# Kernel tuning notes

Measured on AMD Instinct MI355X. Metric: run time of the kernel, lower is better.

## Reference

```python
import jax, jax.numpy as jnp
import numpy as np

D_STATE = 16; D_MODEL = 256; N_HEADS = 8; N_LAYERS = 4; D_REL = 64
HEALTH = 0
WORLD = (1024.0, 1024.0)
B, T, N = 32, 512, 8
ACTION_DIM = 12


def setup_inputs() -> dict:
    key = jax.random.key(0)
    ks = iter(jax.random.split(key, 48))
    s = 0.02
    def w(shape):
        return jax.random.normal(next(ks), shape, jnp.float32) * s
    inp = dict(
        state=jax.random.normal(next(ks), (B, T, N, D_STATE), jnp.float32),
        pos=jax.random.uniform(next(ks), (B, T, N, 2), jnp.float32),
        vel=jax.random.normal(next(ks), (B, T, N, 2), jnp.float32),
        team_ids=jax.random.randint(next(ks), (B, T, N), 0, 2, jnp.int32),
        alive=jax.random.randint(next(ks), (B, T, N), 0, 2, jnp.int32).astype(bool),
        dead=jnp.zeros((D_STATE,), jnp.float32),
        enc_W1=w((D_STATE, D_MODEL)), enc_b1=jnp.zeros((D_MODEL,), jnp.float32),
        enc_W2=w((D_MODEL, D_MODEL)), enc_b2=jnp.zeros((D_MODEL,), jnp.float32),
        team_emb=w((2, D_MODEL)), ship_emb=w((8, D_MODEL)),
        trunk_W1=w((6, D_REL)), trunk_b1=jnp.zeros((D_REL,), jnp.float32),
        trunk_W2=w((D_REL, D_REL)), trunk_b2=jnp.zeros((D_REL,), jnp.float32),
        adapt_W=w((N_LAYERS, D_REL, N_HEADS)), adapt_b=jnp.zeros((N_LAYERS, N_HEADS), jnp.float32),
        norm_w=jnp.ones((N_LAYERS, D_MODEL), jnp.float32),
        Wq=w((N_LAYERS, D_MODEL, D_MODEL)), bq=jnp.zeros((N_LAYERS, D_MODEL), jnp.float32),
        Wk=w((N_LAYERS, D_MODEL, D_MODEL)), bk=jnp.zeros((N_LAYERS, D_MODEL), jnp.float32),
        Wv=w((N_LAYERS, D_MODEL, D_MODEL)), bv=jnp.zeros((N_LAYERS, D_MODEL), jnp.float32),
        Wo=w((N_LAYERS, D_MODEL, D_MODEL)), bo=jnp.zeros((N_LAYERS, D_MODEL), jnp.float32),
        head_W=w((D_MODEL, ACTION_DIM)), head_b=jnp.zeros((ACTION_DIM,), jnp.float32),
    )
    return inp


def _rms(x, g, eps=1e-6):
    return x * jax.lax.rsqrt(jnp.mean(x * x, axis=-1, keepdims=True) + eps) * g


def reference(state, pos, vel, team_ids, alive, dead,
              enc_W1, enc_b1, enc_W2, enc_b2, team_emb, ship_emb,
              trunk_W1, trunk_b1, trunk_W2, trunk_b2, adapt_W, adapt_b,
              norm_w, Wq, bq, Wk, bk, Wv, bv, Wo, bo, head_W, head_b):
    ws = jnp.asarray(WORLD, state.dtype)
    # replace dead entities' state with learned 'dead' vector
    state = jnp.where(alive[..., None], state, dead)
    # state encoder (MLP)
    h = jax.nn.silu(state @ enc_W1 + enc_b1) @ enc_W2 + enc_b2
    # special embeddings
    h = h + team_emb[team_ids] + ship_emb[jnp.arange(N)]  # ship_emb broadcasts over B,T
    # relational trunk: pairwise toroidal geometry features [B,T,N,N,6]
    p = pos * ws
    rel = p[:, :, :, None, :] - p[:, :, None, :, :]
    rel = rel - jnp.round(rel / ws) * ws  # toroidal wrap
    relv = vel[:, :, :, None, :] - vel[:, :, None, :, :]
    dn = jnp.sqrt(jnp.sum(rel * rel, axis=-1) + 1e-8) / ws[0]
    feats = jnp.concatenate([rel / ws, relv, dn[..., None], 1.0 / (1.0 + dn[..., None])], axis=-1)
    trunk = jax.nn.silu(feats @ trunk_W1 + trunk_b1) @ trunk_W2 + trunk_b2  # [B,T,N,N,D_REL]
    dh = D_MODEL // N_HEADS
    scale = dh ** -0.5
    kmask = alive[:, :, None, None, :]  # mask keys
    x = h
    for i in range(N_LAYERS):
        nx = _rms(x, norm_w[i])
        # adapter: per-layer relational bias [B,T,H,N,N]
        bias = jnp.transpose(trunk @ adapt_W[i] + adapt_b[i], (0, 1, 4, 2, 3))
        q = (nx @ Wq[i] + bq[i]).reshape(B, T, N, N_HEADS, dh)
        k = (nx @ Wk[i] + bk[i]).reshape(B, T, N, N_HEADS, dh)
        v = (nx @ Wv[i] + bv[i]).reshape(B, T, N, N_HEADS, dh)
        sc = jnp.einsum('btihd,btjhd->bthij', q, k) * scale + bias
        sc = jnp.where(kmask, sc, -1e9)
        a = jax.nn.softmax(sc, axis=-1)
        o = jnp.einsum('bthij,btjhd->btihd', a, v).reshape(B, T, N, D_MODEL)
        x = x + o @ Wo[i] + bo[i]
    action_logits = x @ head_W + head_b  # [B,T,N,12]
    return action_logits
```

## Files before the change

### kernel.cpp

```cpp
#include <hip/hip_runtime.h>
#include <cstdint>

#define DEV __device__ __forceinline__

typedef __attribute__((ext_vector_type(8))) short short8;
typedef __attribute__((ext_vector_type(4))) float floatx4;
typedef unsigned short u16;
typedef unsigned int u32;

DEV u16 f2bf(float f) {
    unsigned u = __float_as_uint(f);
    return (u16)((u + 0x7fffu + ((u >> 16) & 1u)) >> 16);
}
DEV void unpack2(u32 u, float& a, float& b) {
    a = __uint_as_float(u << 16);
    b = __uint_as_float(u & 0xffff0000u);
}
DEV u32 pack2f(float a, float b) { return (u32)f2bf(a) | ((u32)f2bf(b) << 16); }
DEV float sigm(float x) { return 1.0f / (1.0f + __expf(-x)); }

#define NAG 8
#define DM 256
#define NL 4
#define AD 12
#define MROWS 64
#define NBLK 2048
#define THREADS 512

#define OFF_E1   0
#define OFF_E2   8192
#define OFF_QKVO 73728
#define OFF_TW2  1122304
#define OFF_ADW  1126400
#define WS_TOTAL 1128448
#define WS_BYTES (WS_TOTAL * 2)

#define L_R1    0
#define L_KB    33792
#define L_V     67584
#define L_R2    101376
#define L_RED   135168
#define L_SPOS  137216
#define L_SVEL  137728
#define SMEM_BYTES 138240

#define TRK(row, col) ((row) * 64 + ((((col) >> 3) ^ ((row) & 7)) << 3) + ((col) & 7))

enum { I_STATE=0, I_POS, I_VEL, I_TEAM, I_ALIVE, I_DEAD, I_EW1, I_EB1, I_EW2, I_EB2,
       I_TEMB, I_SEMB, I_TW1, I_TB1, I_TW2, I_TB2, I_ADW, I_ADB, I_NORMW,
       I_WQ, I_BQ, I_WK, I_BK, I_WV, I_BV, I_WO, I_BO, I_HW, I_HB, N_IN };

struct Args { const void* in[N_IN]; float* out; };

__global__ __launch_bounds__(256) void prep_kernel(Args a, u16* ws)
{
    int e = blockIdx.x * 256 + threadIdx.x;
    int mat = blockIdx.y;
    int size, offs, N, Kreal;
    const float* src;
    if (mat == 0)      { size = 8192;  offs = OFF_E1;  N = 256; Kreal = 16;  src = (const float*)a.in[I_EW1]; }
    else if (mat == 1) { size = 65536; offs = OFF_E2;  N = 256; Kreal = 256; src = (const float*)a.in[I_EW2]; }
    else if (mat < 18) {
        int q = mat - 2, l = q >> 2, m = q & 3;
        int wi = (m == 0) ? I_WQ : (m == 1) ? I_WK : (m == 2) ? I_WV : I_WO;
        size = 65536; offs = OFF_QKVO + q * 65536; N = 256; Kreal = 256;
        src = (const float*)a.in[wi] + l * 65536;
    }
    else if (mat == 18) { size = 4096; offs = OFF_TW2; N = 64; Kreal = 64; src = (const float*)a.in[I_TW2]; }
    else                { size = 2048; offs = OFF_ADW; N = 32; Kreal = 64; src = (const float*)a.in[I_ADW]; }
    if (e >= size) return;
    int ksblk = N * 32;
    int ks = e / ksblk, rem = e % ksblk;
    int n = rem >> 5, quad = (rem >> 3) & 3, j = rem & 7;
    int k = ks * 32 + quad * 8 + j;
    float v = 0.0f;
    if (k < Kreal) {
        if (mat == 19) v = src[((n >> 3) * 64 + k) * 8 + (n & 7)];
        else           v = src[k * N + n];
    }
    ws[offs + e] = f2bf(v);
}

DEV short8 ld_u4(const u16* p) {
    return __builtin_bit_cast(short8, *(const uint4*)p);
}
DEV short8 ld_afrag(const u16* A, int stride, int row0, int kofs, int l15, int quad) {
    return ld_u4(A + (row0 + l15) * stride + kofs + quad * 8);
}
DEV short8 ld_bws(const u16* w, int ksblk, int ks, int col, int l15, int quad) {
    return ld_u4(w + ks * ksblk + (col + l15) * 32 + quad * 8);
}
DEV short8 ld_bf32(const float* W, int N, int Kreal, int ks, int col, int l15, int quad) {
    short8 r;
    #pragma unroll
    for (int j = 0; j < 8; j++) {
        int k = ks * 32 + quad * 8 + j;
        float v = (k < Kreal) ? W[k * N + col + l15] : 0.0f;
        r[j] = (short)f2bf(v);
    }
    return r;
}

template<bool UW>
DEV void gemm64(const u16* A, const u16* wsW, const float* Wf,
                int Kb, int Kreal, int colw, int l15, int quad, floatx4 acc[4][2]) {
    #pragma unroll 2
    for (int ks = 0; ks < Kb; ks++) {
        short8 af[4];
        #pragma unroll
        for (int mi = 0; mi < 4; mi++)
            af[mi] = ld_afrag(A, 264, mi * 16, ks * 32, l15, quad);
        short8 bf[2];
        #pragma unroll
        for (int nj = 0; nj < 2; nj++)
            bf[nj] = UW ? ld_bws(wsW, 8192, ks, colw + nj * 16, l15, quad)
                        : ld_bf32(Wf, 256, Kreal, ks, colw + nj * 16, l15, quad);
        #pragma unroll
        for (int mi = 0; mi < 4; mi++)
            #pragma unroll
            for (int nj = 0; nj < 2; nj++)
                acc[mi][nj] = __builtin_amdgcn_mfma_f32_16x16x32_bf16(af[mi], bf[nj], acc[mi][nj], 0, 0, 0);
    }
}

template<bool UW>
__global__ __launch_bounds__(THREADS, 2) void yemong_mfma(Args a, const u16* ws)
{
    extern __shared__ char smem[];
    u16* sR1   = (u16*)(smem + L_R1);
    u16* skb   = (u16*)(smem + L_KB);
    u16* sV    = (u16*)(smem + L_V);
    u16* sR2   = (u16*)(smem + L_R2);
    float* sred = (float*)(smem + L_RED);
    float* spos = (float*)(smem + L_SPOS);
    float* svel = (float*)(smem + L_SVEL);

    const int t = threadIdx.x, bid = blockIdx.x;
    const int lane = t & 63, w = t >> 6;
    const int l15 = lane & 15, quad = lane >> 4;
    const int colw = w * 32;
    const int rowt = w * 64;
    const int p = w >> 1, h0 = (w & 1) * 4;

    float xr[4][2][4];
    u32 br[NL][4][2];
    u32 amask;

    unsigned mp = 0;
    const unsigned* au = (const unsigned*)a.in[I_ALIVE];
    #pragma unroll
    for (int i = 0; i < 16; i++) mp |= au[i];
    const bool abyte = (mp > 1u);
    auto aliveAt = [&](int r) -> int {
        int gi = bid * MROWS + r;
        return abyte ? (int)((const unsigned char*)a.in[I_ALIVE])[gi]
                     : ((const int*)a.in[I_ALIVE])[gi];
    };
    auto rms_partials = [&]() {
        float ssv[16];
        #pragma unroll
        for (int mi = 0; mi < 4; mi++)
            #pragma unroll
            for (int r = 0; r < 4; r++) {
                float x0 = xr[mi][0][r], x1 = xr[mi][1][r];
                ssv[mi * 4 + r] = fmaf(x0, x0, x1 * x1);
            }
        #pragma unroll
        for (int m = 1; m < 16; m <<= 1)
            #pragma unroll
            for (int k2 = 0; k2 < 16; k2++) ssv[k2] += __shfl_xor(ssv[k2], m);
        if (l15 == 0) {
            #pragma unroll
            for (int mi = 0; mi < 4; mi++)
                #pragma unroll
                for (int r = 0; r < 4; r++)
                    sred[(mi * 16 + quad * 4 + r) * 8 + w] = ssv[mi * 4 + r];
        }
    };

    if (t < 128) {
        int n = t >> 1, d = t & 1;
        spos[n * 2 + d] = ((const float*)a.in[I_POS])[(bid * MROWS + n) * 2 + d] * 1024.0f;
        svel[n * 2 + d] = ((const float*)a.in[I_VEL])[(bid * MROWS + n) * 2 + d];
    }
    {
        int tk = 2 * p + (quad >> 1);
        amask = 0;
        #pragma unroll
        for (int j = 0; j < 8; j++) amask |= (aliveAt(tk * 8 + j) ? 1u : 0u) << j;
    }
    {
        const float* gs = (const float*)a.in[I_STATE];
        const float* gd = (const float*)a.in[I_DEAD];
        #pragma unroll
        for (int it = 0; it < 4; it++) {
            int idx = t + THREADS * it;
            int r = idx >> 5, kk = idx & 31;
            float v = 0.0f;
            if (kk < 16) v = aliveAt(r) ? gs[(bid * MROWS + r) * 16 + kk] : gd[kk];
            sR2[r * 264 + kk] = f2bf(v);
        }
    }
    __syncthreads();

    {
        floatx4 acc[4][2] = {};
        gemm64<UW>(sR2, ws + OFF_E1, (const float*)a.in[I_EW1], 1, 16, colw, l15, quad, acc);
        __syncthreads();
        const float* b1 = (const float*)a.in[I_EB1];
        #pragma unroll
        for (int nj = 0; nj < 2; nj++) {
            int c = colw + nj * 16 + l15;
            float bb = b1[c];
            #pragma unroll
            for (int mi = 0; mi < 4; mi++)
                #pragma unroll
                for (int r = 0; r < 4; r++) {
                    float v = acc[mi][nj][r] + bb;
                    sR2[(mi * 16 + quad * 4 + r) * 264 + c] = f2bf(v * sigm(v));
                }
        }
    }
    __syncthreads();

    {
        floatx4 acc[4][2] = {};
        gemm64<UW>(sR2, ws + OFF_E2, (const float*)a.in[I_EW2], 8, 256, colw, l15, quad, acc);
        const float* b2 = (const float*)a.in[I_EB2];
        const float* te = (const float*)a.in[I_TEMB];
        const float* se = (const float*)a.in[I_SEMB];
        const int* gteam = (const int*)a.in[I_TEAM];
        int team16[16];
        #pragma unroll
        for (int mi = 0; mi < 4; mi++)
            #pragma unroll
            for (int r = 0; r < 4; r++)
                team16[mi * 4 + r] = gteam[bid * MROWS + mi * 16 + quad * 4 + r];
        #pragma unroll
        for (int nj = 0; nj < 2; nj++) {
            int c = colw + nj * 16 + l15;
            float bb = b2[c];
            #pragma unroll
            for (int mi = 0; mi < 4; mi++)
                #pragma unroll
                for (int r = 0; r < 4; r++) {
                    int row = mi * 16 + quad * 4 + r;
                    xr[mi][nj][r] = acc[mi][nj][r] + bb + te[team16[mi * 4 + r] * 256 + c] + se[(row & 7) * 256 + c];
                }
        }
        rms_partials();
    }

    {
        int tokp = t >> 6;
        int pi = tokp * 8 + ((t >> 3) & 7), pj = tokp * 8 + (t & 7);
        float rx = spos[pi * 2 + 0] - spos[pj * 2 + 0];
        float ry = spos[pi * 2 + 1] - spos[pj * 2 + 1];
        rx -= rintf(rx * (1.0f / 1024.0f)) * 1024.0f;
        ry -= rintf(ry * (1.0f / 1024.0f)) * 1024.0f;
        float vx = svel[pi * 2 + 0] - svel[pj * 2 + 0];
        float vy = svel[pi * 2 + 1] - svel[pj * 2 + 1];
        float dn = sqrtf(rx * rx + ry * ry + 1e-8f) * (1.0f / 1024.0f);
        float f[6] = {rx * (1.0f / 1024.0f), ry * (1.0f / 1024.0f), vx, vy, dn, 1.0f / (1.0f + dn)};
        const float* W1 = (const float*)a.in[I_TW1];
        const float* B1 = (const float*)a.in[I_TB1];
        #pragma unroll
        for (int g = 0; g < 8; g++) {
            float v[8];
            #pragma unroll
            for (int e = 0; e < 8; e++) v[e] = B1[g * 8 + e];
            #pragma unroll
            for (int kk = 0; kk < 6; kk++)
                #pragma unroll
                for (int e = 0; e < 8; e++) v[e] = fmaf(f[kk], W1[kk * 64 + g * 8 + e], v[e]);
            #pragma unroll
            for (int e = 0; e < 8; e++) v[e] = v[e] * sigm(v[e]);
            uint4 pk;
            pk.x = pack2f(v[0], v[1]); pk.y = pack2f(v[2], v[3]);
            pk.z = pack2f(v[4], v[5]); pk.w = pack2f(v[6], v[7]);
            *(uint4*)&sR1[t * 64 + ((g ^ (t & 7)) << 3)] = pk;
        }
    }
    __syncthreads();

    {
        short8 taf[4][2];
        #pragma unroll
        for (int mi = 0; mi < 4; mi++)
            #pragma unroll
            for (int ks = 0; ks < 2; ks++) {
                int R = rowt + mi * 16 + l15;
                taf[mi][ks] = ld_u4(&sR1[R * 64 + (((ks * 4 + quad) ^ (R & 7)) << 3)]);
            }
        floatx4 tacc[4][4] = {};
        #pragma unroll
        for (int ks = 0; ks < 2; ks++) {
            short8 bf[4];
            #pragma unroll
            for (int nj = 0; nj < 4; nj++)
                bf[nj] = UW ? ld_bws(ws + OFF_TW2, 2048, ks, nj * 16, l15, quad)
                            : ld_bf32((const float*)a.in[I_TW2], 64, 64, ks, nj * 16, l15, quad);
            #pragma unroll
            for (int mi = 0; mi < 4; mi++)
                #pragma unroll
                for (int nj = 0; nj < 4; nj++)
                    tacc[mi][nj] = __builtin_amdgcn_mfma_f32_16x16x32_bf16(taf[mi][ks], bf[nj], tacc[mi][nj], 0, 0, 0);
        }
        const float* B2 = (const float*)a.in[I_TB2];
        #pragma unroll
        for (int nj = 0; nj < 4; nj++) {
            int c = nj * 16 + l15;
            float bb = B2[c];
            #pragma unroll
            for (int mi = 0; mi < 4; mi++)
                #pragma unroll
                for (int r = 0; r < 4; r++) {
                    int row = rowt + mi * 16 + quad * 4 + r;
                    sR1[TRK(row, c)] = f2bf(tacc[mi][nj][r] + bb);
                }
        }
    }
    __syncthreads();

    {
        floatx4 tacc[4][2] = {};
        #pragma unroll
        for (int ks = 0; ks < 2; ks++) {
            short8 bf[2];
            #pragma unroll
            for (int nj = 0; nj < 2; nj++) {
                if (UW) bf[nj] = ld_bws(ws + OFF_ADW, 1024, ks, nj * 16, l15, quad);
                else {
                    const float* adw = (const float*)a.in[I_ADW];
                    int n = nj * 16 + l15;
                    #pragma unroll
                    for (int j = 0; j < 8; j++) {
                        int k = ks * 32 + quad * 8 + j;
                        bf[nj][j] = (short)f2bf(k < 64 ? adw[((n >> 3) * 64 + k) * 8 + (n & 7)] : 0.0f);
                    }
                }
            }
            #pragma unroll
            for (int mi = 0; mi < 4; mi++) {
                int R = rowt + mi * 16 + l15;
                short8 af = ld_u4(&sR1[R * 64 + (((ks * 4 + quad) ^ (R & 7)) << 3)]);
                #pragma unroll
                for (int nj = 0; nj < 2; nj++)
                    tacc[mi][nj] = __builtin_amdgcn_mfma_f32_16x16x32_bf16(af, bf[nj], tacc[mi][nj], 0, 0, 0);
            }
        }
        const float* adb = (const float*)a.in[I_ADB];
        #pragma unroll
        for (int nj = 0; nj < 2; nj++) {
            int n = nj * 16 + l15;
            float bb = adb[n];
            #pragma unroll
            for (int mi = 0; mi < 4; mi++)
                #pragma unroll
                for (int r = 0; r < 4; r++) {
                    int pl = mi * 16 + quad * 4 + r;
                    sR2[((w * 4 + (n >> 3)) * 8 + (n & 7)) * 64 + pl] = f2bf(tacc[mi][nj][r] + bb);
                }
        }
        __syncthreads();
        int tk = 2 * p + (quad >> 1);
        #pragma unroll
        for (int l = 0; l < NL; l++)
            #pragma unroll
            for (int u = 0; u < 4; u++) {
                int base = ((tk * 4 + l) * 8 + (h0 + u)) * 64 + (l15 & 7) * 8 + (quad & 1) * 4;
                const u32* bp = (const u32*)&sR2[base];
                br[l][u][0] = bp[0];
                br[l][u][1] = bp[1];
            }
    }
    __syncthreads();

    const float* normw = (const float*)a.in[I_NORMW];
    const bool qvalid = ((quad >> 1) == (l15 >> 3));
    #pragma unroll
    for (int l = 0; l < NL; l++) {
        {
            float invr[16];
            #pragma unroll
            for (int mi = 0; mi < 4; mi++)
                #pragma unroll
                for (int r = 0; r < 4; r++) {
                    int row = mi * 16 + quad * 4 + r;
                    float4 pa = *(const float4*)&sred[row * 8];
                    float4 pb = *(const float4*)&sred[row * 8 + 4];
                    float s = pa.x + pa.y + pa.z + pa.w + pb.x + pb.y + pb.z + pb.w;
                    invr[mi * 4 + r] = rsqrtf(s * (1.0f / 256.0f) + 1e-6f);
                }
            #pragma unroll
            for (int nj = 0; nj < 2; nj++) {
                int c = colw + nj * 16 + l15;
                float nwv = normw[l * 256 + c];
                #pragma unroll
                for (int mi = 0; mi < 4; mi++)
                    #pragma unroll
                    for (int r = 0; r < 4; r++)
                        sR2[(mi * 16 + quad * 4 + r) * 264 + c] = f2bf(xr[mi][nj][r] * invr[mi * 4 + r] * nwv);
            }
        }
        __syncthreads();

        {
            const float* bqf = (const float*)a.in[I_BQ] + l * 256;
            const float* bkf = (const float*)a.in[I_BK] + l * 256;
            const float* bvf = (const float*)a.in[I_BV] + l * 256;
            {
                floatx4 acc[4][2] = {};
                gemm64<UW>(sR2, ws + OFF_QKVO + (l * 4 + 0) * 65536, (const float*)a.in[I_WQ] + l * 65536, 8, 256, colw, l15, quad, acc);
                #pragma unroll
                for (int nj = 0; nj < 2; nj++) {
                    int c = colw + nj * 16 + l15;
                    float bb = bqf[c];
                    #pragma unroll
                    for (int mi = 0; mi < 4; mi++)
                        #pragma unroll
                        for (int r = 0; r < 4; r++)
                            sR1[(mi * 16 + quad * 4 + r) * 264 + c] = f2bf((acc[mi][nj][r] + bb) * 0.17677669529663689f);
                }
            }
            {
                floatx4 acc[4][2] = {};
                gemm64<UW>(sR2, ws + OFF_QKVO + (l * 4 + 1) * 65536, (const float*)a.in[I_WK] + l * 65536, 8, 256, colw, l15, quad, acc);
                #pragma unroll
                for (int nj = 0; nj < 2; nj++) {
                    int c = colw + nj * 16 + l15;
                    float bb = bkf[c];
                    #pragma unroll
                    for (int mi = 0; mi < 4; mi++)
                        #pragma unroll
                        for (int r = 0; r < 4; r++)
                            skb[(mi * 16 + quad * 4 + r) * 264 + c] = f2bf(acc[mi][nj][r] + bb);
                }
            }
            {
                floatx4 acc[4][2] = {};
                gemm64<UW>(sR2, ws + OFF_QKVO + (l * 4 + 2) * 65536, (const float*)a.in[I_WV] + l * 65536, 8, 256, colw, l15, quad, acc);
                #pragma unroll
                for (int nj = 0; nj < 2; nj++) {
                    int c = colw + nj * 16 + l15;
                    float bb = bvf[c];
                    #pragma unroll
                    for (int mi = 0; mi < 4; mi++)
                        #pragma unroll
                        for (int r = 0; r < 4; r++)
                            sV[(mi * 16 + quad * 4 + r) * 264 + c] = f2bf(acc[mi][nj][r] + bb);
                }
            }
        }
        __syncthreads();

        {
            short8 kf[4], qf[4];
            #pragma unroll
            for (int u = 0; u < 4; u++) {
                int h = h0 + u;
                kf[u] = ld_u4(&skb[(p * 16 + l15) * 264 + h * 32 + quad * 8]);
                qf[u] = ld_u4(&sR1[(p * 16 + l15) * 264 + h * 32 + quad * 8]);
            }
            floatx4 st[4];
            #pragma unroll
            for (int u = 0; u < 4; u++) {
                floatx4 zero = {};
                st[u] = __builtin_amdgcn_mfma_f32_16x16x32_bf16(kf[u], qf[u], zero, 0, 0, 0);
            }
            short8 paf[4];
            #pragma unroll
            for (int u = 0; u < 4; u++) {
                float bb[4];
                unpack2(br[l][u][0], bb[0], bb[1]);
                unpack2(br[l][u][1], bb[2], bb[3]);
                float s[4];
                #pragma unroll
                for (int r = 0; r < 4; r++) {
                    int jl = (quad & 1) * 4 + r;
                    bool alv = (amask >> jl) & 1;
                    s[r] = qvalid ? (alv ? st[u][r] + bb[r] : -1.0e9f) : -2.0e9f;
                }
                float mx = fmaxf(fmaxf(s[0], s[1]), fmaxf(s[2], s[3]));
                mx = fmaxf(mx, __shfl_xor(mx, 16));
                mx = fmaxf(mx, __shfl_xor(mx, 32));
                float e[4], sm = 0.0f;
                #pragma unroll
                for (int r = 0; r < 4; r++) { e[r] = __expf(s[r] - mx); sm += e[r]; }
                sm += __shfl_xor(sm, 16);
                sm += __shfl_xor(sm, 32);
                float inv = 1.0f / sm;
                u32 u01 = pack2f(e[0] * inv, e[1] * inv);
                u32 u23 = pack2f(e[2] * inv, e[3] * inv);
                int srcA = (quad * 32 + l15) & 63;
                u32 a0 = (u32)__shfl((int)u01, srcA);
                u32 a1 = (u32)__shfl((int)u23, srcA);
                u32 a2 = (u32)__shfl((int)u01, (srcA + 16) & 63);
                u32 a3 = (u32)__shfl((int)u23, (srcA + 16) & 63);
                if (quad >= 2) { a0 = 0; a1 = 0; a2 = 0; a3 = 0; }
                uint4 tmp; tmp.x = a0; tmp.y = a1; tmp.z = a2; tmp.w = a3;
                paf[u] = __builtin_bit_cast(short8, tmp);
            }
            #pragma unroll
            for (int u = 0; u < 4; u++) {
                int h = h0 + u;
                #pragma unroll
                for (int nt = 0; nt < 2; nt++) {
                    short8 vf;
                    if (quad < 2) {
                        #pragma unroll
                        for (int jj = 0; jj < 8; jj++) {
                            int kr = quad * 8 + jj;
                            vf[jj] = (short)sV[(p * 16 + kr) * 264 + h * 32 + nt * 16 + l15];
                        }
                    } else {
                        #pragma unroll
                        for (int jj = 0; jj < 8; jj++) vf[jj] = 0;
                    }
                    floatx4 z2 = {};
                    floatx4 o = __builtin_amdgcn_mfma_f32_16x16x32_bf16(paf[u], vf, z2, 0, 0, 0);
                    #pragma unroll
                    for (int r = 0; r < 4; r++)
                        sR1[(p * 16 + quad * 4 + r) * 264 + h * 32 + nt * 16 + l15] = f2bf(o[r]);
                }
            }
        }
        __syncthreads();

        {
            floatx4 acc[4][2] = {};
            gemm64<UW>(sR1, ws + OFF_QKVO + (l * 4 + 3) * 65536, (const float*)a.in[I_WO] + l * 65536,
                       8, 256, colw, l15, quad, acc);
            const float* bo = (const float*)a.in[I_BO] + l * 256;
            #pragma unroll
            for (int nj = 0; nj < 2; nj++) {
                float bb = bo[colw + nj * 16 + l15];
                #pragma unroll
                for (int mi = 0; mi < 4; mi++)
                    #pragma unroll
                    for (int r = 0; r < 4; r++)
                        xr[mi][nj][r] += acc[mi][nj][r] + bb;
            }
            rms_partials();
        }
        __syncthreads();
    }

    {
        float* xf = (float*)sR1;
        #pragma unroll
        for (int nj = 0; nj < 2; nj++) {
            int c = colw + nj * 16 + l15;
            #pragma unroll
            for (int mi = 0; mi < 4; mi++)
                #pragma unroll
                for (int r = 0; r < 4; r++)
                    xf[(mi * 16 + quad * 4 + r) * 264 + c] = xr[mi][nj][r];
        }
        __syncthreads();
        int row = t >> 3, pp = t & 7;
        const float* HW = (const float*)a.in[I_HW];
        float ah[12];
        #pragma unroll
        for (int c = 0; c < 12; c++) ah[c] = 0.0f;
        for (int kk = pp * 32; kk < pp * 32 + 32; kk++) {
            float xv = xf[row * 264 + kk];
            #pragma unroll
            for (int c = 0; c < 12; c++) ah[c] = fmaf(xv, HW[kk * 12 + c], ah[c]);
        }
        #pragma unroll
        for (int c = 0; c < 12; c++) {
            ah[c] += __shfl_xor(ah[c], 1);
            ah[c] += __shfl_xor(ah[c], 2);
            ah[c] += __shfl_xor(ah[c], 4);
        }
        if (pp == 0) {
            const float* hb = (const float*)a.in[I_HB];
            #pragma unroll
            for (int c = 0; c < 12; c++)
                a.out[(bid * MROWS + row) * AD + c] = ah[c] + hb[c];
        }
    }
}

extern "C" void kernel_launch(void* const* d_in, const int* in_sizes, int n_in,
                              void* d_out, int out_size, void* d_ws, size_t ws_size,
                              hipStream_t stream) {
    (void)in_sizes; (void)n_in; (void)out_size;
    Args a;
    for (int i = 0; i < N_IN; i++) a.in[i] = d_in[i];
    a.out = (float*)d_out;
    u16* ws16 = (u16*)d_ws;
    const bool use_ws = (ws_size >= (size_t)WS_BYTES) && (d_ws != nullptr);
    if (use_ws) {
        hipLaunchKernelGGL(prep_kernel, dim3(256, 20), dim3(256), 0, stream, a, ws16);
        hipFuncSetAttribute((const void*)yemong_mfma<true>, hipFuncAttributeMaxDynamicSharedMemorySize, SMEM_BYTES);
        hipLaunchKernelGGL((yemong_mfma<true>), dim3(NBLK), dim3(THREADS), SMEM_BYTES, stream, a, ws16);
    } else {
        hipFuncSetAttribute((const void*)yemong_mfma<false>, hipFuncAttributeMaxDynamicSharedMemorySize, SMEM_BYTES);
        hipLaunchKernelGGL((yemong_mfma<false>), dim3(NBLK), dim3(THREADS), SMEM_BYTES, stream, a, ws16);
    }
}
```

Before: 981.5 us.

## Store V transposed in LDS, use packed bf16 conversion, deepen GEMM unroll

```diff
diff --git a/kernel.cpp b/kernel.cpp
--- a/kernel.cpp
+++ b/kernel.cpp
@@ -1,4 +1,5 @@
 #include <hip/hip_runtime.h>
+#include <hip/hip_bf16.h>
 #include <cstdint>
 
 #define DEV __device__ __forceinline__
@@ -16,7 +17,13 @@
     a = __uint_as_float(u << 16);
     b = __uint_as_float(u & 0xffff0000u);
 }
-DEV u32 pack2f(float a, float b) { return (u32)f2bf(a) | ((u32)f2bf(b) << 16); }
+DEV u32 cvt2(float a, float b) {
+    float2 f; f.x = a; f.y = b;
+    __hip_bfloat162 h = __float22bfloat162_rn(f);
+    u32 r;
+    __builtin_memcpy(&r, &h, 4);
+    return r;
+}
 DEV float sigm(float x) { return 1.0f / (1.0f + __expf(-x)); }
 
 #define NAG 8
@@ -37,12 +44,12 @@
 
 #define L_R1    0
 #define L_KB    33792
-#define L_V     67584
-#define L_R2    101376
-#define L_RED   135168
-#define L_SPOS  137216
-#define L_SVEL  137728
-#define SMEM_BYTES 138240
+#define L_VT    67584
+#define L_R2    104576
+#define L_RED   138368
+#define L_SPOS  140416
+#define L_SVEL  140928
+#define SMEM_BYTES 141440
 
 #define TRK(row, col) ((row) * 64 + ((((col) >> 3) ^ ((row) & 7)) << 3) + ((col) & 7))
 
@@ -104,7 +111,7 @@
 template<bool UW>
 DEV void gemm64(const u16* A, const u16* wsW, const float* Wf,
                 int Kb, int Kreal, int colw, int l15, int quad, floatx4 acc[4][2]) {
-    #pragma unroll 2
+    #pragma unroll 4
     for (int ks = 0; ks < Kb; ks++) {
         short8 af[4];
         #pragma unroll
@@ -129,7 +136,7 @@
     extern __shared__ char smem[];
     u16* sR1   = (u16*)(smem + L_R1);
     u16* skb   = (u16*)(smem + L_KB);
-    u16* sV    = (u16*)(smem + L_V);
+    u16* sVT   = (u16*)(smem + L_VT);
     u16* sR2   = (u16*)(smem + L_R2);
     float* sred = (float*)(smem + L_RED);
     float* spos = (float*)(smem + L_SPOS);
@@ -213,12 +220,15 @@
             int c = colw + nj * 16 + l15;
             float bb = b1[c];
             #pragma unroll
-            for (int mi = 0; mi < 4; mi++)
-                #pragma unroll
-                for (int r = 0; r < 4; r++) {
-                    float v = acc[mi][nj][r] + bb;
-                    sR2[(mi * 16 + quad * 4 + r) * 264 + c] = f2bf(v * sigm(v));
-                }
+            for (int mi = 0; mi < 4; mi++) {
+                float v0 = acc[mi][nj][0] + bb, v1 = acc[mi][nj][1] + bb;
+                float v2 = acc[mi][nj][2] + bb, v3 = acc[mi][nj][3] + bb;
+                u32 lo = cvt2(v0 * sigm(v0), v1 * sigm(v1));
+                u32 hi = cvt2(v2 * sigm(v2), v3 * sigm(v3));
+                u16* b = &sR2[(mi * 16 + quad * 4) * 264 + c];
+                b[0] = (u16)lo; b[264] = (u16)(lo >> 16);
+                b[528] = (u16)hi; b[792] = (u16)(hi >> 16);
+            }
         }
     }
     __syncthreads();
@@ -276,8 +286,8 @@
             #pragma unroll
             for (int e = 0; e < 8; e++) v[e] = v[e] * sigm(v[e]);
             uint4 pk;
-            pk.x = pack2f(v[0], v[1]); pk.y = pack2f(v[2], v[3]);
-            pk.z = pack2f(v[4], v[5]); pk.w = pack2f(v[6], v[7]);
+            pk.x = cvt2(v[0], v[1]); pk.y = cvt2(v[2], v[3]);
+            pk.z = cvt2(v[4], v[5]); pk.w = cvt2(v[6], v[7]);
             *(uint4*)&sR1[t * 64 + ((g ^ (t & 7)) << 3)] = pk;
         }
     }
@@ -397,10 +407,13 @@
                 int c = colw + nj * 16 + l15;
                 float nwv = normw[l * 256 + c];
                 #pragma unroll
-                for (int mi = 0; mi < 4; mi++)
-                    #pragma unroll
-                    for (int r = 0; r < 4; r++)
-                        sR2[(mi * 16 + quad * 4 + r) * 264 + c] = f2bf(xr[mi][nj][r] * invr[mi * 4 + r] * nwv);
+                for (int mi = 0; mi < 4; mi++) {
+                    u32 lo = cvt2(xr[mi][nj][0] * invr[mi * 4 + 0] * nwv, xr[mi][nj][1] * invr[mi * 4 + 1] * nwv);
+                    u32 hi = cvt2(xr[mi][nj][2] * invr[mi * 4 + 2] * nwv, xr[mi][nj][3] * invr[mi * 4 + 3] * nwv);
+                    u16* b = &sR2[(mi * 16 + quad * 4) * 264 + c];
+                    b[0] = (u16)lo; b[264] = (u16)(lo >> 16);
+                    b[528] = (u16)hi; b[792] = (u16)(hi >> 16);
+                }
             }
         }
         __syncthreads();
@@ -417,10 +430,13 @@
                     int c = colw + nj * 16 + l15;
                     float bb = bqf[c];
                     #pragma unroll
-                    for (int mi = 0; mi < 4; mi++)
-                        #pragma unroll
-                        for (int r = 0; r < 4; r++)
-                            sR1[(mi * 16 + quad * 4 + r) * 264 + c] = f2bf((acc[mi][nj][r] + bb) * 0.17677669529663689f);
+                    for (int mi = 0; mi < 4; mi++) {
+                        u32 lo = cvt2((acc[mi][nj][0] + bb) * 0.17677669529663689f, (acc[mi][nj][1] + bb) * 0.17677669529663689f);
+                        u32 hi = cvt2((acc[mi][nj][2] + bb) * 0.17677669529663689f, (acc[mi][nj][3] + bb) * 0.17677669529663689f);
+                        u16* b = &sR1[(mi * 16 + quad * 4) * 264 + c];
+                        b[0] = (u16)lo; b[264] = (u16)(lo >> 16);
+                        b[528] = (u16)hi; b[792] = (u16)(hi >> 16);
+                    }
                 }
             }
             {
@@ -431,10 +447,13 @@
                     int c = colw + nj * 16 + l15;
                     float bb = bkf[c];
                     #pragma unroll
-                    for (int mi = 0; mi < 4; mi++)
-                        #pragma unroll
-                        for (int r = 0; r < 4; r++)
-                            skb[(mi * 16 + quad * 4 + r) * 264 + c] = f2bf(acc[mi][nj][r] + bb);
+                    for (int mi = 0; mi < 4; mi++) {
+                        u32 lo = cvt2(acc[mi][nj][0] + bb, acc[mi][nj][1] + bb);
+                        u32 hi = cvt2(acc[mi][nj][2] + bb, acc[mi][nj][3] + bb);
+                        u16* b = &skb[(mi * 16 + quad * 4) * 264 + c];
+                        b[0] = (u16)lo; b[264] = (u16)(lo >> 16);
+                        b[528] = (u16)hi; b[792] = (u16)(hi >> 16);
+                    }
                 }
             }
             {
@@ -445,10 +464,12 @@
                     int c = colw + nj * 16 + l15;
                     float bb = bvf[c];
                     #pragma unroll
-                    for (int mi = 0; mi < 4; mi++)
-                        #pragma unroll
-                        for (int r = 0; r < 4; r++)
-                            sV[(mi * 16 + quad * 4 + r) * 264 + c] = f2bf(acc[mi][nj][r] + bb);
+                    for (int mi = 0; mi < 4; mi++) {
+                        uint2 pk;
+                        pk.x = cvt2(acc[mi][nj][0] + bb, acc[mi][nj][1] + bb);
+                        pk.y = cvt2(acc[mi][nj][2] + bb, acc[mi][nj][3] + bb);
+                        *(uint2*)&sVT[c * 72 + mi * 16 + quad * 4] = pk;
+                    }
                 }
             }
         }
@@ -490,8 +511,8 @@
                 sm += __shfl_xor(sm, 16);
                 sm += __shfl_xor(sm, 32);
                 float inv = 1.0f / sm;
-                u32 u01 = pack2f(e[0] * inv, e[1] * inv);
-                u32 u23 = pack2f(e[2] * inv, e[3] * inv);
+                u32 u01 = cvt2(e[0] * inv, e[1] * inv);
+                u32 u23 = cvt2(e[2] * inv, e[3] * inv);
                 int srcA = (quad * 32 + l15) & 63;
                 u32 a0 = (u32)__shfl((int)u01, srcA);
                 u32 a1 = (u32)__shfl((int)u23, srcA);
@@ -508,20 +529,18 @@
                 for (int nt = 0; nt < 2; nt++) {
                     short8 vf;
                     if (quad < 2) {
-                        #pragma unroll
-                        for (int jj = 0; jj < 8; jj++) {
-                            int kr = quad * 8 + jj;
-                            vf[jj] = (short)sV[(p * 16 + kr) * 264 + h * 32 + nt * 16 + l15];
-                        }
+                        vf = ld_u4(&sVT[(h * 32 + nt * 16 + l15) * 72 + p * 16 + quad * 8]);
                     } else {
-                        #pragma unroll
-                        for (int jj = 0; jj < 8; jj++) vf[jj] = 0;
+                        uint4 z = {};
+                        vf = __builtin_bit_cast(short8, z);
                     }
                     floatx4 z2 = {};
                     floatx4 o = __builtin_amdgcn_mfma_f32_16x16x32_bf16(paf[u], vf, z2, 0, 0, 0);
-                    #pragma unroll
-                    for (int r = 0; r < 4; r++)
-                        sR1[(p * 16 + quad * 4 + r) * 264 + h * 32 + nt * 16 + l15] = f2bf(o[r]);
+                    u32 lo = cvt2(o[0], o[1]);
+                    u32 hi = cvt2(o[2], o[3]);
+                    u16* ob = &sR1[(p * 16 + quad * 4) * 264 + h * 32 + nt * 16 + l15];
+                    ob[0] = (u16)lo; ob[264] = (u16)(lo >> 16);
+                    ob[528] = (u16)hi; ob[792] = (u16)(hi >> 16);
                 }
             }
         }
@@ -594,10 +613,10 @@
     const bool use_ws = (ws_size >= (size_t)WS_BYTES) && (d_ws != nullptr);
     if (use_ws) {
         hipLaunchKernelGGL(prep_kernel, dim3(256, 20), dim3(256), 0, stream, a, ws16);
-        hipFuncSetAttribute((const void*)yemong_mfma<true>, hipFuncAttributeMaxDynamicSharedMemorySize, SMEM_BYTES);
+        (void)hipFuncSetAttribute((const void*)yemong_mfma<true>, hipFuncAttributeMaxDynamicSharedMemorySize, SMEM_BYTES);
         hipLaunchKernelGGL((yemong_mfma<true>), dim3(NBLK), dim3(THREADS), SMEM_BYTES, stream, a, ws16);
     } else {
-        hipFuncSetAttribute((const void*)yemong_mfma<false>, hipFuncAttributeMaxDynamicSharedMemorySize, SMEM_BYTES);
+        (void)hipFuncSetAttribute((const void*)yemong_mfma<false>, hipFuncAttributeMaxDynamicSharedMemorySize, SMEM_BYTES);
         hipLaunchKernelGGL((yemong_mfma<false>), dim3(NBLK), dim3(THREADS), SMEM_BYTES, stream, a, ws16);
     }
 }
```

After: 964.1 us. Within noise of the previous version (-1.8%).
